# Optimization experiments

Measured on AMD Instinct MI355X. Metric: run time of the kernel, lower is better.

The kernel has to match this reference:

```python
import math
import jax, jax.numpy as jnp
import numpy as np

DIM = 4096
N_HEADS = 32
N_KV_HEADS = 8
HEAD_DIM = DIM // N_HEADS        # 128
N_REP = N_HEADS // N_KV_HEADS    # 4
BSZ = 1
SEQ = 2048
ROPE_THETA = 500000.0


def setup_inputs() -> dict:
    key = jax.random.key(0)
    ks = jax.random.split(key, 5)
    scale = 1.0 / math.sqrt(DIM)
    x = jax.random.normal(ks[0], (BSZ, SEQ, DIM), dtype=jnp.float32)
    wq = jax.random.normal(ks[1], (N_HEADS * HEAD_DIM, DIM), dtype=jnp.float32) * scale
    wk = jax.random.normal(ks[2], (N_KV_HEADS * HEAD_DIM, DIM), dtype=jnp.float32) * scale
    wv = jax.random.normal(ks[3], (N_KV_HEADS * HEAD_DIM, DIM), dtype=jnp.float32) * scale
    wo = jax.random.normal(ks[4], (N_HEADS * HEAD_DIM, DIM), dtype=jnp.float32).T * scale
    wo = jnp.asarray(wo)  # [DIM, N_HEADS*HEAD_DIM] like nn.Linear(in=heads*hd, out=dim).weight
    # RoPE tables: freqs_cis[t, j] = exp(i * t * theta^{-2j/head_dim}), j in [0, head_dim/2)
    inv_freq = 1.0 / (ROPE_THETA ** (np.arange(0, HEAD_DIM, 2, dtype=np.float32) / HEAD_DIM))
    t = np.arange(SEQ, dtype=np.float32)
    ang = np.outer(t, inv_freq)  # [SEQ, HEAD_DIM//2]
    freqs_cos = jnp.asarray(np.cos(ang), dtype=jnp.float32)
    freqs_sin = jnp.asarray(np.sin(ang), dtype=jnp.float32)
    # additive causal mask [SEQ, SEQ]
    mask = jnp.where(jnp.tril(jnp.ones((SEQ, SEQ), dtype=bool)), 0.0, -1e9).astype(jnp.float32)
    return {"x": x, "wq": wq, "wk": wk, "wv": wv, "wo": wo,
            "freqs_cos": freqs_cos, "freqs_sin": freqs_sin, "mask": mask}


def _apply_rope(xh, cos, sin):
    # xh: [b, s, h, head_dim]; cos/sin: [s, head_dim//2]
    b, s, h, d = xh.shape
    xr = xh.reshape(b, s, h, d // 2, 2)
    x0, x1 = xr[..., 0], xr[..., 1]
    c = cos[None, :, None, :]
    sn = sin[None, :, None, :]
    o0 = x0 * c - x1 * sn
    o1 = x0 * sn + x1 * c
    return jnp.stack([o0, o1], axis=-1).reshape(b, s, h, d)


def reference(x, wq, wk, wv, wo, freqs_cos, freqs_sin, mask):
    bsz, seqlen, _ = x.shape
    xq = (x @ wq.T).reshape(bsz, seqlen, N_HEADS, HEAD_DIM)
    xk = (x @ wk.T).reshape(bsz, seqlen, N_KV_HEADS, HEAD_DIM)
    xv = (x @ wv.T).reshape(bsz, seqlen, N_KV_HEADS, HEAD_DIM)
    xq = _apply_rope(xq, freqs_cos, freqs_sin)
    xk = _apply_rope(xk, freqs_cos, freqs_sin)
    # repeat_kv (GQA expansion)
    keys = jnp.repeat(xk, N_REP, axis=2)    # [b, s, N_HEADS, hd]
    values = jnp.repeat(xv, N_REP, axis=2)
    scores = jnp.einsum('bqhd,bkhd->bhqk', xq, keys) / math.sqrt(HEAD_DIM)
    scores = scores + mask[None, None, :, :]
    scores = jax.nn.softmax(scores.astype(jnp.float32), axis=-1).astype(xq.dtype)
    out = jnp.einsum('bhqk,bkhd->bqhd', scores, values)
    out = out.reshape(bsz, seqlen, N_HEADS * HEAD_DIM)
    return out @ wo.T
```

## Files before the change

### kernel.cpp

```cpp
#include <hip/hip_runtime.h>
#include <math.h>
#include <stdint.h>
#include <stddef.h>


typedef __attribute__((ext_vector_type(8))) short bf16x8;
typedef __attribute__((ext_vector_type(4))) short bf16x4;
typedef __attribute__((ext_vector_type(4))) float f32x4;
typedef unsigned short u16;
typedef unsigned int u32;

#define NEG_BIG (-1.0e9f)
#define MFMA32(a, b, c) __builtin_amdgcn_mfma_f32_16x16x32_bf16(a, b, c, 0, 0, 0)
#define SFENCE() __builtin_amdgcn_sched_barrier(0)
#define BAR() __builtin_amdgcn_s_barrier()
#define VMW(n_) asm volatile("s_waitcnt vmcnt(" #n_ ")" ::: "memory")

__device__ __forceinline__ float bf2f(u16 b) {
    return __uint_as_float(((unsigned int)b) << 16);
}
__device__ __forceinline__ u16 f2bf(float f) {
    unsigned int u = __float_as_uint(f);
    u += 0x7fff + ((u >> 16) & 1);
    return (u16)(u >> 16);
}
__device__ __forceinline__ void gld_lds16(short* lds, const u16* g) {
    __builtin_amdgcn_global_load_lds(
        (const __attribute__((address_space(1))) void*)g,
        (__attribute__((address_space(3))) void*)lds, 16, 0, 0);
}

__global__ __launch_bounds__(256) void cvt_all(
    const float* __restrict__ x, const float* __restrict__ wq,
    const float* __restrict__ wk, const float* __restrict__ wv,
    const float* __restrict__ wo,
    u16* __restrict__ xb, u16* __restrict__ wqb, u16* __restrict__ wkb,
    u16* __restrict__ wvb, u16* __restrict__ wob) {
    const int b = blockIdx.x;
    const float* s; u16* d; int off;
    if (b < 4096)       { s = x;  d = xb;  off = b; }
    else if (b < 12288) { s = wq; d = wqb; off = b - 4096; }
    else if (b < 14336) { s = wk; d = wkb; off = b - 12288; }
    else if (b < 16384) { s = wv; d = wvb; off = b - 14336; }
    else                { s = wo; d = wob; off = b - 16384; }
    const int i = off * 2048 + threadIdx.x * 8;
    float4 a, c;
    __builtin_memcpy(&a, s + i, 16);
    __builtin_memcpy(&c, s + i + 4, 16);
    bf16x8 o;
    o[0] = (short)f2bf(a.x); o[1] = (short)f2bf(a.y);
    o[2] = (short)f2bf(a.z); o[3] = (short)f2bf(a.w);
    o[4] = (short)f2bf(c.x); o[5] = (short)f2bf(c.y);
    o[6] = (short)f2bf(c.z); o[7] = (short)f2bf(c.w);
    __builtin_memcpy(d + i, &o, 16);
}


#define QSTGA(bf_, ks_, kt_)                                                 \
    { _Pragma("unroll") for (int r_ = 0; r_ < 2; ++r_)                       \
        gld_lds16(Ad + (bf_) * 16384 + (ks_) * 8192 + r_ * 4096,             \
                  Ag + gK * r_ + (size_t)(kt_) * 64 + (ks_) * 32); }
#define QSTGB(bf_, ks_, kt_)                                                 \
    { _Pragma("unroll") for (int r_ = 0; r_ < 2; ++r_)                       \
        gld_lds16(Bd + (bf_) * 16384 + (ks_) * 8192 + r_ * 4096,             \
                  Bg + gK * r_ + (size_t)(kt_) * 64 + (ks_) * 32); }
#define QRDA(bank_, bf_, ks_, mh_)                                           \
    { _Pragma("unroll") for (int i_ = 0; i_ < 4; ++i_)                       \
        __builtin_memcpy(&bank_[i_], S + (bf_) * 16384 + (ks_) * 8192 +      \
                         abase + ((mh_) * 64 + i_ * 16) * 32, 16); }
#define QRDB(bank_, bf_, ks_)                                                \
    { _Pragma("unroll") for (int n_ = 0; n_ < 4; ++n_)                       \
        __builtin_memcpy(&bank_[n_], Bs + (bf_) * 16384 + (ks_) * 8192 +     \
                         bbase + n_ * 512, 16); }
#define QMM(afb_, bfb_, mh_)                                                 \
    {                                                                        \
        __builtin_amdgcn_s_setprio(1);                                       \
        _Pragma("unroll") for (int i_ = 0; i_ < 4; ++i_)                     \
            _Pragma("unroll") for (int n_ = 0; n_ < 4; ++n_)                 \
                acc[(mh_) * 4 + i_][n_] =                                    \
                    MFMA32(afb_[i_], bfb_[n_], acc[(mh_) * 4 + i_][n_]);     \
        __builtin_amdgcn_s_setprio(0);                                       \
    }

template <int OUT>
__device__ __forceinline__ void gemm_q(const u16* __restrict__ A,
                                       const u16* __restrict__ B,
                                       void* __restrict__ C,
                                       int mb, int nb, int N, int K,
                                       short* __restrict__ S) {
    short* const Bs = S + 32768;
    const int t = threadIdx.x;
    const int lane = t & 63, l15 = lane & 15, quad = lane >> 4;
    const int wid = t >> 6, wr = wid >> 2, wc = wid & 3;

    const int srow = t >> 2;
    const int cs = (t & 3) ^ ((t >> 3) & 3);
    const u16* const Ag = A + (size_t)(mb * 256 + srow) * K + cs * 8;
    const u16* const Bg = B + (size_t)(nb * 256 + srow) * K + cs * 8;
    short* const Ad = S + t * 8;
    short* const Bd = Bs + t * 8;
    const size_t gK = (size_t)128 * K;

    const int swz = (quad ^ ((l15 >> 1) & 3)) * 8;
    const int abase = (wr * 128 + l15) * 32 + swz;
    const int bbase = (wc * 64 + l15) * 32 + swz;

    f32x4 acc[8][4] = {};
    bf16x8 af0[4], af1[4], bf0[4], bf1[4];

    QSTGA(0, 0, 0); QSTGB(0, 0, 0);
    QSTGA(0, 1, 0); QSTGB(0, 1, 0);
    QSTGA(1, 0, 1); QSTGB(1, 0, 1);
    VMW(8);
    BAR();
    QRDA(af0, 0, 0, 0); QRDB(bf0, 0, 0);
    SFENCE();

    const int nIt = K >> 7;
    for (int it = 0; it < nIt - 1; ++it) {
        const int k1 = 2 * it + 1, kn0 = 2 * it + 2, kn1 = 2 * it + 3;
        QSTGA(1, 1, k1);  QRDA(af1, 0, 0, 1);                    QMM(af0, bf0, 0); SFENCE(); VMW(6); BAR();
        QSTGB(1, 1, k1);  QRDA(af0, 0, 1, 0); QRDB(bf1, 0, 1);   QMM(af1, bf0, 1); SFENCE();         BAR();
        QSTGA(0, 0, kn0); QRDA(af1, 0, 1, 1);                    QMM(af0, bf1, 0); SFENCE(); VMW(6); BAR();
        QSTGB(0, 0, kn0); QRDA(af0, 1, 0, 0); QRDB(bf0, 1, 0);   QMM(af1, bf1, 1); SFENCE();         BAR();
        QSTGA(0, 1, kn0); QRDA(af1, 1, 0, 1);                    QMM(af0, bf0, 0); SFENCE(); VMW(6); BAR();
        QSTGB(0, 1, kn0); QRDA(af0, 1, 1, 0); QRDB(bf1, 1, 1);   QMM(af1, bf0, 1); SFENCE();         BAR();
        QSTGA(1, 0, kn1); QRDA(af1, 1, 1, 1);                    QMM(af0, bf1, 0); SFENCE(); VMW(6); BAR();
        QSTGB(1, 0, kn1); QRDA(af0, 0, 0, 0); QRDB(bf0, 0, 0);   QMM(af1, bf1, 1); SFENCE();         BAR();
    }
    {
        const int k1 = 2 * nIt - 1;
        QSTGA(1, 1, k1);  QRDA(af1, 0, 0, 1);                    QMM(af0, bf0, 0); SFENCE(); VMW(6); BAR();
        QSTGB(1, 1, k1);  QRDA(af0, 0, 1, 0); QRDB(bf1, 0, 1);   QMM(af1, bf0, 1); SFENCE();         BAR();
        QRDA(af1, 0, 1, 1);                                      QMM(af0, bf1, 0); SFENCE(); VMW(4); BAR();
        QRDA(af0, 1, 0, 0); QRDB(bf0, 1, 0);                     QMM(af1, bf1, 1); SFENCE();         BAR();
        QRDA(af1, 1, 0, 1);                                      QMM(af0, bf0, 0); SFENCE(); VMW(0); BAR();
        QRDA(af0, 1, 1, 0); QRDB(bf1, 1, 1);                     QMM(af1, bf0, 1); SFENCE();         BAR();
        QRDA(af1, 1, 1, 1);                                      QMM(af0, bf1, 0); SFENCE();         BAR();
        QMM(af1, bf1, 1);
    }

#pragma unroll
    for (int i8 = 0; i8 < 8; ++i8) {
        const int rowb = mb * 256 + wr * 128 + (i8 >> 2) * 64 +
                         (i8 & 3) * 16 + quad * 4;
#pragma unroll
        for (int j = 0; j < 4; ++j) {
            const int col = nb * 256 + wc * 64 + j * 16 + l15;
            if (OUT == 2) {
                bf16x4 v;
#pragma unroll
                for (int r = 0; r < 4; ++r) v[r] = (short)f2bf(acc[i8][j][r]);
                __builtin_memcpy((u16*)C + (size_t)col * 2048 + rowb, &v, 8);
            } else {
#pragma unroll
                for (int r = 0; r < 4; ++r)
                    ((u16*)C)[(size_t)(rowb + r) * N + col] =
                        f2bf(acc[i8][j][r]);
            }
        }
    }
}

__global__ __launch_bounds__(512, 2) void qkv_proj8(
    const u16* __restrict__ x,
    const u16* __restrict__ wq, const u16* __restrict__ wk,
    const u16* __restrict__ wv,
    u16* __restrict__ Q, u16* __restrict__ Kc, u16* __restrict__ Vt) {
    __shared__ __align__(16) short S[65536];
    const int lid = blockIdx.x;
    const int swzb = (lid & 7) * 24 + (lid >> 3);
    const int mb = swzb & 7, y = swzb >> 3;
    if (y < 16)
        gemm_q<0>(x, wq, Q, mb, y, 4096, 4096, S);
    else if (y < 20)
        gemm_q<0>(x, wk, Kc, mb, y - 16, 1024, 4096, S);
    else
        gemm_q<2>(x, wv, Vt, mb, y - 20, 1024, 4096, S);
}


#define O8_STG(bf_, ks_, kt_)                                                \
    {                                                                        \
        gld_lds16(Ad + (bf_) * 8192 + (ks_) * 4096,                          \
                  Ag + (size_t)(kt_) * 64 + (ks_) * 32);                     \
        _Pragma("unroll") for (int r_ = 0; r_ < 2; ++r_)                     \
            gld_lds16(Bd + (bf_) * 16384 + (ks_) * 8192 + r_ * 4096,         \
                      Bg + gK * r_ + (size_t)(kt_) * 64 + (ks_) * 32);       \
    }
#define O8_PHASE(bf_, ks_, STAGE_, WAIT_)                                    \
    {                                                                        \
        _Pragma("unroll") for (int n_ = 0; n_ < 4; ++n_)                     \
            __builtin_memcpy(&bfr[n_], Bs + (bf_) * 16384 + (ks_) * 8192 +   \
                                           bbase + n_ * 512, 16);            \
        _Pragma("unroll") for (int i_ = 0; i_ < 4; ++i_)                     \
            __builtin_memcpy(&af[i_], S + (bf_) * 8192 + (ks_) * 4096 +      \
                                          abase + i_ * 512, 16);             \
        STAGE_;                                                              \
        SFENCE();                                                            \
        __builtin_amdgcn_s_barrier();                                        \
        asm volatile("s_waitcnt lgkmcnt(0)" ::: "memory");                   \
        SFENCE();                                                            \
        __builtin_amdgcn_s_setprio(1);                                       \
        _Pragma("unroll") for (int i_ = 0; i_ < 4; ++i_)                     \
            _Pragma("unroll") for (int n_ = 0; n_ < 4; ++n_)                 \
                acc[i_][n_] = MFMA32(af[i_], bfr[n_], acc[i_][n_]);          \
        __builtin_amdgcn_s_setprio(0);                                       \
        SFENCE();                                                            \
        WAIT_;                                                               \
        __builtin_amdgcn_s_barrier();                                        \
    }

__global__ __launch_bounds__(512, 2) void oproj8(
    const u16* __restrict__ A, const u16* __restrict__ wo,
    float* __restrict__ out) {
    __shared__ __align__(16) short S[49152];
    short* const Bs = S + 16384;
    const int lid = blockIdx.x;
    const int logical = (lid & 7) * 32 + (lid >> 3);
    const int mb = logical & 15, nb = logical >> 4;

    const int t = threadIdx.x;
    const int lane = t & 63, l15 = lane & 15, quad = lane >> 4;
    const int wid = t >> 6, wr = wid >> 2, wc = wid & 3;

    const int srow = t >> 2;
    const int cs = (t & 3) ^ ((t >> 3) & 3);
    const u16* const Ag = A + (size_t)(mb * 128 + srow) * 4096 + cs * 8;
    const u16* const Bg = wo + (size_t)(nb * 256 + srow) * 4096 + cs * 8;
    short* const Ad = S + t * 8;
    short* const Bd = Bs + t * 8;
    const size_t gK = (size_t)128 * 4096;

    const int swz = (quad ^ ((l15 >> 1) & 3)) * 8;
    const int abase = (wr * 64 + l15) * 32 + swz;
    const int bbase = (wc * 64 + l15) * 32 + swz;

    f32x4 acc[4][4] = {};
    bf16x8 af[4], bfr[4];

    O8_STG(0, 0, 0); O8_STG(0, 1, 0); O8_STG(1, 0, 1);
    VMW(6);
    BAR();

    const int nIt = 32;
    for (int it = 0; it < nIt - 1; ++it) {
        const int k1 = 2 * it + 1, kn0 = 2 * it + 2, kn1 = 2 * it + 3;
        O8_PHASE(0, 0, O8_STG(1, 1, k1),  VMW(6));
        O8_PHASE(0, 1, O8_STG(0, 0, kn0), VMW(6));
        O8_PHASE(1, 0, O8_STG(0, 1, kn0), VMW(6));
        O8_PHASE(1, 1, O8_STG(1, 0, kn1), VMW(6));
    }
    {
        const int k1 = 2 * nIt - 1;
        O8_PHASE(0, 0, O8_STG(1, 1, k1), VMW(6));
        O8_PHASE(0, 1, ,                 VMW(3));
        O8_PHASE(1, 0, ,                 VMW(0));
        O8_PHASE(1, 1, , );
    }

#pragma unroll
    for (int i = 0; i < 4; ++i) {
        const int rowb = mb * 128 + wr * 64 + i * 16 + quad * 4;
#pragma unroll
        for (int j = 0; j < 4; ++j) {
            const int col = nb * 256 + wc * 64 + j * 16 + l15;
#pragma unroll
            for (int r = 0; r < 4; ++r)
                out[(size_t)(rowb + r) * 4096 + col] = acc[i][j][r];
        }
    }
}

__global__ __launch_bounds__(256) void rope_all(
    u16* __restrict__ Q, u16* __restrict__ Kc,
    const float* __restrict__ cosb, const float* __restrict__ sinb) {
    const int idx = blockIdx.x * blockDim.x + threadIdx.x;
    const int i = idx & 63;
    const int hh = (idx >> 6) % 40;
    const int s = (idx >> 6) / 40;
    u16* p;
    if (hh < 32)
        p = Q + (size_t)s * 4096 + hh * 128 + 2 * i;
    else
        p = Kc + (size_t)s * 1024 + (hh - 32) * 128 + 2 * i;
    const float x0 = bf2f(p[0]), x1 = bf2f(p[1]);
    const float c = cosb[s * 64 + i], sn = sinb[s * 64 + i];
    p[0] = f2bf(x0 * c - x1 * sn);
    p[1] = f2bf(x0 * sn + x1 * c);
}

__device__ __forceinline__ int kswz(int row, int cs) {
    int f = (row & 3) | ((row & 8) >> 1);
    return row * 128 + ((cs ^ f) << 3);
}

template <bool MASKED>
__device__ __forceinline__ void fa_step_lds(
    const short* __restrict__ Kl, const short* __restrict__ Vl,
    int kb, int kadd, int q0, int l15, int quad,
    const int (&koff)[8], const int (&voff)[8],
    const bf16x8 (&qf)[4], const bf16x8 vones,
    f32x4 (&o)[8], f32x4& o9, float& m) {
    const float c1 = 0.08838834764831845f * 1.4426950408889634f;

    bf16x8 kf[8];
#pragma unroll
    for (int i = 0; i < 8; ++i)
        __builtin_memcpy(&kf[i], Kl + koff[i] + kadd, 16);
    f32x4 s0 = {0, 0, 0, 0}, s1 = {0, 0, 0, 0};
#pragma unroll
    for (int c = 0; c < 4; ++c) {
        s0 = MFMA32(kf[c], qf[c], s0);
        s1 = MFMA32(kf[4 + c], qf[c], s1);
    }

    bf16x8 vf[8];
#pragma unroll
    for (int n = 0; n < 8; ++n) __builtin_memcpy(&vf[n], Vl + voff[n], 16);

    float sv0[4], sv1[4];
    const int q = q0 + l15;
#pragma unroll
    for (int r = 0; r < 4; ++r) {
        sv0[r] = s0[r];
        sv1[r] = s1[r];
        if (MASKED) {
            if (kb + 8 * quad + r > q) sv0[r] = NEG_BIG;
            if (kb + 8 * quad + 4 + r > q) sv1[r] = NEG_BIG;
        }
    }

    float mx = fmaxf(fmaxf(fmaxf(sv0[0], sv0[1]), fmaxf(sv0[2], sv0[3])),
                     fmaxf(fmaxf(sv1[0], sv1[1]), fmaxf(sv1[2], sv1[3])));
    mx = fmaxf(mx, __shfl_xor(mx, 16));
    mx = fmaxf(mx, __shfl_xor(mx, 32));

    if (!__all(mx <= m + 90.0f)) {
        float mnew = fmaxf(m, mx);
        float alpha = exp2f((m - mnew) * c1);
        float aO[4];
#pragma unroll
        for (int r = 0; r < 4; ++r) aO[r] = __shfl(alpha, quad * 20 + r);
#pragma unroll
        for (int n = 0; n < 8; ++n)
#pragma unroll
            for (int r = 0; r < 4; ++r) o[n][r] *= aO[r];
#pragma unroll
        for (int r = 0; r < 4; ++r) o9[r] *= aO[r];
        m = mnew;
    }

    const float mc = m * c1;
    float p0[4], p1[4];
#pragma unroll
    for (int r = 0; r < 4; ++r) {
        p0[r] = exp2f(__builtin_fmaf(sv0[r], c1, -mc));
        p1[r] = exp2f(__builtin_fmaf(sv1[r], c1, -mc));
    }

    u32 w0, w1, w2, w3;
    asm("v_cvt_pk_bf16_f32 %0, %1, %2" : "=v"(w0) : "v"(p0[0]), "v"(p0[1]));
    asm("v_cvt_pk_bf16_f32 %0, %1, %2" : "=v"(w1) : "v"(p0[2]), "v"(p0[3]));
    asm("v_cvt_pk_bf16_f32 %0, %1, %2" : "=v"(w2) : "v"(p1[0]), "v"(p1[1]));
    asm("v_cvt_pk_bf16_f32 %0, %1, %2" : "=v"(w3) : "v"(p1[2]), "v"(p1[3]));
    u32 wa[4] = {w0, w1, w2, w3};
    bf16x8 pa;
    __builtin_memcpy(&pa, wa, 16);

#pragma unroll
    for (int n = 0; n < 8; ++n) o[n] = MFMA32(pa, vf[n], o[n]);
    o9 = MFMA32(pa, vones, o9);
}

__device__ __forceinline__ void fa_task(
    const u16* __restrict__ Q, const u16* __restrict__ Kc,
    const u16* __restrict__ Vt, u16* __restrict__ O,
    short* __restrict__ Kl0, short* __restrict__ Vl0,
    int q0, int nbt64, int h, int kvh, int t) {
    const int lane = t & 63;
    const int l15 = lane & 15, quad = lane >> 4;

    bf16x8 qf[4];
    const u16* qp = Q + (size_t)(q0 + l15) * 4096 + h * 128 + quad * 8;
#pragma unroll
    for (int c = 0; c < 4; ++c) __builtin_memcpy(&qf[c], qp + c * 32, 16);

    bf16x8 vones;
#pragma unroll
    for (int i = 0; i < 8; ++i) vones[i] = (short)0x3F80;

    const u16* ksrc[4]; short* kdst[4];
    const u16* vsrc[4]; short* vdst[4];
#pragma unroll
    for (int r = 0; r < 4; ++r) {
        int row = (t >> 4) + 16 * r;
        int slot = t & 15;
        int f = (row & 3) | ((row & 8) >> 1);
        int cks = slot ^ f;
        ksrc[r] = Kc + (size_t)row * 1024 + kvh * 128 + cks * 8;
        kdst[r] = Kl0 + (t + 256 * r) * 8;
        int rowv = (t >> 3) + 32 * r;
        int csv = (t & 7) ^ ((t >> 3) & 7);
        vsrc[r] = Vt + (size_t)(kvh * 128 + rowv) * 2048 + csv * 8;
        vdst[r] = Vl0 + (t + 256 * r) * 8;
    }

    const int rk0 = 8 * (l15 >> 2) + (l15 & 3);
    int koff[8], voff0[8], voff1[8];
#pragma unroll
    for (int c = 0; c < 4; ++c) {
        koff[c] = kswz(rk0, quad + c * 4);
        koff[4 + c] = kswz(rk0 + 4, quad + c * 4);
    }
#pragma unroll
    for (int n = 0; n < 8; ++n) {
        const int row = n * 16 + l15;
        voff0[n] = row * 64 + ((quad ^ (l15 & 7)) << 3);
        voff1[n] = row * 64 + (((quad + 4) ^ (l15 & 7)) << 3);
    }

    f32x4 o[8] = {};
    f32x4 o9 = {0, 0, 0, 0};
    float m = NEG_BIG;
    const int my_nb32 = (q0 + 47) / 32;

#pragma unroll
    for (int r = 0; r < 4; ++r) {
        gld_lds16(kdst[r], ksrc[r]);
        gld_lds16(vdst[r], vsrc[r]);
    }
    __syncthreads();

    for (int ib = 0; ib < nbt64; ++ib) {
        if (ib + 1 < nbt64) {
            const int kb = (ib + 1) * 64;
            const int bo = ((ib + 1) & 1) * 8192;
#pragma unroll
            for (int r = 0; r < 4; ++r) {
                gld_lds16(kdst[r] + bo, ksrc[r] + (size_t)kb * 1024);
                gld_lds16(vdst[r] + bo, vsrc[r] + kb);
            }
        }
        const short* Kl = Kl0 + (ib & 1) * 8192;
        const short* Vl = Vl0 + (ib & 1) * 8192;
#pragma unroll
        for (int sub = 0; sub < 2; ++sub) {
            const int ib32 = 2 * ib + sub;
            if (ib32 < my_nb32) {
                const int kb = ib * 64 + sub * 32;
                const int kadd = sub * 4096;
                if (ib32 == my_nb32 - 1)
                    fa_step_lds<true>(Kl, Vl, kb, kadd, q0, l15, quad, koff,
                                      sub ? voff1 : voff0, qf, vones, o, o9,
                                      m);
                else
                    fa_step_lds<false>(Kl, Vl, kb, kadd, q0, l15, quad, koff,
                                       sub ? voff1 : voff0, qf, vones, o, o9,
                                       m);
            }
        }
        __syncthreads();
    }

    float inv[4];
#pragma unroll
    for (int r = 0; r < 4; ++r) inv[r] = 1.f / o9[r];
#pragma unroll
    for (int n = 0; n < 8; ++n)
#pragma unroll
        for (int r = 0; r < 4; ++r) {
            int row = q0 + quad * 4 + r;
            O[(size_t)row * 4096 + h * 128 + n * 16 + l15] =
                f2bf(o[n][r] * inv[r]);
        }
}

__global__ __launch_bounds__(256, 2) void flash_attn(
    const u16* __restrict__ Q, const u16* __restrict__ Kc,
    const u16* __restrict__ Vt, u16* __restrict__ O) {
    __shared__ __align__(16) short Kl[2 * 64 * 128];
    __shared__ __align__(16) short Vl[2 * 128 * 64];
    const int pp = blockIdx.x;
    const int h = blockIdx.y;
    const int kvh = h >> 2;
    const int t = threadIdx.x, wave = t >> 6;
    fa_task(Q, Kc, Vt, O, Kl, Vl, pp * 64 + wave * 16, pp + 1, h, kvh, t);
    const int tb = 31 - pp;
    fa_task(Q, Kc, Vt, O, Kl, Vl, tb * 64 + (3 - wave) * 16, tb + 1, h,
            kvh, t);
}

extern "C" void kernel_launch(void* const* d_in, const int* in_sizes, int n_in,
                              void* d_out, int out_size, void* d_ws,
                              size_t ws_size, hipStream_t stream) {
    const float* x  = (const float*)d_in[0];
    const float* wq = (const float*)d_in[1];
    const float* wk = (const float*)d_in[2];
    const float* wv = (const float*)d_in[3];
    const float* wo = (const float*)d_in[4];
    const float* fc = (const float*)d_in[5];
    const float* fs = (const float*)d_in[6];
    float* out = (float*)d_out;

    const int NX = 2048 * 4096;
    const int NQW = 4096 * 4096;
    const int NKW = 1024 * 4096;
    const int NKV = 2048 * 1024;

    u16* Q   = (u16*)d_ws;
    u16* Kc  = Q   + NX;
    u16* Vt  = Kc  + NKV;
    u16* Ao  = Vt  + NKV;
    u16* xb  = Ao  + NX;
    u16* wqb = xb  + NX;
    u16* wkb = wqb + NQW;
    u16* wvb = wkb + NKW;
    u16* wob = wvb + NKW;

    cvt_all<<<24576, 256, 0, stream>>>(x, wq, wk, wv, wo,
                                       xb, wqb, wkb, wvb, wob);
    qkv_proj8<<<192, 512, 0, stream>>>(xb, wqb, wkb, wvb, Q, Kc, Vt);
    rope_all<<<20480, 256, 0, stream>>>(Q, Kc, fc, fs);
    flash_attn<<<dim3(16, 32), 256, 0, stream>>>(Q, Kc, Vt, Ao);
    oproj8<<<256, 512, 0, stream>>>(Ao, wob, out);
}
```

Baseline: 471.4 us.

## Retile QKV GEMM warps to 4x2 grid with 64x128 per-wave tiles

Changes the per-wave tile of the QKV projection GEMM from 128x64 (2x4 wave grid) to 64x128 (4x2 wave grid), loading 4 A and 8 B fragments per k-step. It also merges the A/B staging and LDS reads into four half-phases per iteration instead of eight, which halves the number of barriers and waitcnts. The goal is fewer sync points and less LDS read traffic per MFMA. The trade-off is that more B fragments stay live, which raises register pressure and could hurt occupancy at 2 blocks per CU.

New measurement: 552.0 us. +17.1%, slower.

```diff
diff --git a/kernel.cpp b/kernel.cpp
--- a/kernel.cpp
+++ b/kernel.cpp
@@ -64,21 +64,21 @@
     { _Pragma("unroll") for (int r_ = 0; r_ < 2; ++r_)                       \
         gld_lds16(Bd + (bf_) * 16384 + (ks_) * 8192 + r_ * 4096,             \
                   Bg + gK * r_ + (size_t)(kt_) * 64 + (ks_) * 32); }
-#define QRDA(bank_, bf_, ks_, mh_)                                           \
-    { _Pragma("unroll") for (int i_ = 0; i_ < 4; ++i_)                       \
-        __builtin_memcpy(&bank_[i_], S + (bf_) * 16384 + (ks_) * 8192 +      \
-                         abase + ((mh_) * 64 + i_ * 16) * 32, 16); }
-#define QRDB(bank_, bf_, ks_)                                                \
-    { _Pragma("unroll") for (int n_ = 0; n_ < 4; ++n_)                       \
-        __builtin_memcpy(&bank_[n_], Bs + (bf_) * 16384 + (ks_) * 8192 +     \
-                         bbase + n_ * 512, 16); }
-#define QMM(afb_, bfb_, mh_)                                                 \
+#define QRD(ab_, bb_, bf_, ks_)                                              \
+    {                                                                        \
+        _Pragma("unroll") for (int i_ = 0; i_ < 4; ++i_)                     \
+            __builtin_memcpy(&ab_[i_], S + (bf_) * 16384 + (ks_) * 8192 +    \
+                             abase + i_ * 512, 16);                          \
+        _Pragma("unroll") for (int n_ = 0; n_ < 8; ++n_)                     \
+            __builtin_memcpy(&bb_[n_], Bs + (bf_) * 16384 + (ks_) * 8192 +   \
+                             bbase + n_ * 512, 16);                          \
+    }
+#define QMM(ab_, bb_)                                                        \
     {                                                                        \
         __builtin_amdgcn_s_setprio(1);                                       \
         _Pragma("unroll") for (int i_ = 0; i_ < 4; ++i_)                     \
-            _Pragma("unroll") for (int n_ = 0; n_ < 4; ++n_)                 \
-                acc[(mh_) * 4 + i_][n_] =                                    \
-                    MFMA32(afb_[i_], bfb_[n_], acc[(mh_) * 4 + i_][n_]);     \
+            _Pragma("unroll") for (int n_ = 0; n_ < 8; ++n_)                 \
+                acc[i_][n_] = MFMA32(ab_[i_], bb_[n_], acc[i_][n_]);         \
         __builtin_amdgcn_s_setprio(0);                                       \
     }
 
@@ -91,7 +91,7 @@
     short* const Bs = S + 32768;
     const int t = threadIdx.x;
     const int lane = t & 63, l15 = lane & 15, quad = lane >> 4;
-    const int wid = t >> 6, wr = wid >> 2, wc = wid & 3;
+    const int wid = t >> 6, wr = wid >> 1, wc = wid & 1;
 
     const int srow = t >> 2;
     const int cs = (t & 3) ^ ((t >> 3) & 3);
@@ -102,61 +102,57 @@
     const size_t gK = (size_t)128 * K;
 
     const int swz = (quad ^ ((l15 >> 1) & 3)) * 8;
-    const int abase = (wr * 128 + l15) * 32 + swz;
-    const int bbase = (wc * 64 + l15) * 32 + swz;
-
-    f32x4 acc[8][4] = {};
-    bf16x8 af0[4], af1[4], bf0[4], bf1[4];
+    const int abase = (wr * 64 + l15) * 32 + swz;
+    const int bbase = (wc * 128 + l15) * 32 + swz;
+
+    f32x4 acc[4][8] = {};
+    bf16x8 af0[4], af1[4], bf0[8], bf1[8];
 
     QSTGA(0, 0, 0); QSTGB(0, 0, 0);
     QSTGA(0, 1, 0); QSTGB(0, 1, 0);
     QSTGA(1, 0, 1); QSTGB(1, 0, 1);
-    VMW(8);
+    VMW(4);
     BAR();
-    QRDA(af0, 0, 0, 0); QRDB(bf0, 0, 0);
+    QRD(af0, bf0, 0, 0);
     SFENCE();
 
     const int nIt = K >> 7;
     for (int it = 0; it < nIt - 1; ++it) {
         const int k1 = 2 * it + 1, kn0 = 2 * it + 2, kn1 = 2 * it + 3;
-        QSTGA(1, 1, k1);  QRDA(af1, 0, 0, 1);                    QMM(af0, bf0, 0); SFENCE(); VMW(6); BAR();
-        QSTGB(1, 1, k1);  QRDA(af0, 0, 1, 0); QRDB(bf1, 0, 1);   QMM(af1, bf0, 1); SFENCE();         BAR();
-        QSTGA(0, 0, kn0); QRDA(af1, 0, 1, 1);                    QMM(af0, bf1, 0); SFENCE(); VMW(6); BAR();
-        QSTGB(0, 0, kn0); QRDA(af0, 1, 0, 0); QRDB(bf0, 1, 0);   QMM(af1, bf1, 1); SFENCE();         BAR();
-        QSTGA(0, 1, kn0); QRDA(af1, 1, 0, 1);                    QMM(af0, bf0, 0); SFENCE(); VMW(6); BAR();
-        QSTGB(0, 1, kn0); QRDA(af0, 1, 1, 0); QRDB(bf1, 1, 1);   QMM(af1, bf0, 1); SFENCE();         BAR();
-        QSTGA(1, 0, kn1); QRDA(af1, 1, 1, 1);                    QMM(af0, bf1, 0); SFENCE(); VMW(6); BAR();
-        QSTGB(1, 0, kn1); QRDA(af0, 0, 0, 0); QRDB(bf0, 0, 0);   QMM(af1, bf1, 1); SFENCE();         BAR();
+        QSTGA(1, 1, k1);  QSTGB(1, 1, k1);
+        QRD(af1, bf1, 0, 1); QMM(af0, bf0); SFENCE(); VMW(4); BAR();
+        QSTGA(0, 0, kn0); QSTGB(0, 0, kn0);
+        QRD(af0, bf0, 1, 0); QMM(af1, bf1); SFENCE(); VMW(4); BAR();
+        QSTGA(0, 1, kn0); QSTGB(0, 1, kn0);
+        QRD(af1, bf1, 1, 1); QMM(af0, bf0); SFENCE(); VMW(4); BAR();
+        QSTGA(1, 0, kn1); QSTGB(1, 0, kn1);
+        QRD(af0, bf0, 0, 0); QMM(af1, bf1); SFENCE(); VMW(4); BAR();
     }
     {
         const int k1 = 2 * nIt - 1;
-        QSTGA(1, 1, k1);  QRDA(af1, 0, 0, 1);                    QMM(af0, bf0, 0); SFENCE(); VMW(6); BAR();
-        QSTGB(1, 1, k1);  QRDA(af0, 0, 1, 0); QRDB(bf1, 0, 1);   QMM(af1, bf0, 1); SFENCE();         BAR();
-        QRDA(af1, 0, 1, 1);                                      QMM(af0, bf1, 0); SFENCE(); VMW(4); BAR();
-        QRDA(af0, 1, 0, 0); QRDB(bf0, 1, 0);                     QMM(af1, bf1, 1); SFENCE();         BAR();
-        QRDA(af1, 1, 0, 1);                                      QMM(af0, bf0, 0); SFENCE(); VMW(0); BAR();
-        QRDA(af0, 1, 1, 0); QRDB(bf1, 1, 1);                     QMM(af1, bf0, 1); SFENCE();         BAR();
-        QRDA(af1, 1, 1, 1);                                      QMM(af0, bf1, 0); SFENCE();         BAR();
-        QMM(af1, bf1, 1);
-    }
-
-#pragma unroll
-    for (int i8 = 0; i8 < 8; ++i8) {
-        const int rowb = mb * 256 + wr * 128 + (i8 >> 2) * 64 +
-                         (i8 & 3) * 16 + quad * 4;
-#pragma unroll
-        for (int j = 0; j < 4; ++j) {
-            const int col = nb * 256 + wc * 64 + j * 16 + l15;
+        QSTGA(1, 1, k1); QSTGB(1, 1, k1);
+        QRD(af1, bf1, 0, 1); QMM(af0, bf0); SFENCE(); VMW(4); BAR();
+        QRD(af0, bf0, 1, 0); QMM(af1, bf1); SFENCE(); VMW(0); BAR();
+        QRD(af1, bf1, 1, 1); QMM(af0, bf0); SFENCE();         BAR();
+        QMM(af1, bf1);
+    }
+
+#pragma unroll
+    for (int i = 0; i < 4; ++i) {
+        const int rowb = mb * 256 + wr * 64 + i * 16 + quad * 4;
+#pragma unroll
+        for (int n = 0; n < 8; ++n) {
+            const int col = nb * 256 + wc * 128 + n * 16 + l15;
             if (OUT == 2) {
                 bf16x4 v;
 #pragma unroll
-                for (int r = 0; r < 4; ++r) v[r] = (short)f2bf(acc[i8][j][r]);
+                for (int r = 0; r < 4; ++r) v[r] = (short)f2bf(acc[i][n][r]);
                 __builtin_memcpy((u16*)C + (size_t)col * 2048 + rowb, &v, 8);
             } else {
 #pragma unroll
                 for (int r = 0; r < 4; ++r)
                     ((u16*)C)[(size_t)(rowb + r) * N + col] =
-                        f2bf(acc[i8][j][r]);
+                        f2bf(acc[i][n][r]);
             }
         }
     }
```
